# Performance work log

Measured on AMD Instinct MI355X. Metric: run time of the kernel, lower is better.

Reference implementation:

```python
import jax, jax.numpy as jnp
import numpy as np

CPS = 16          # coarse_patch_size = 128 / resolution[0](=8)
ENC = 128         # enc_dim = CPS*CPS/2
LN_EPS = 1e-5


def setup_inputs() -> dict:
    key = jax.random.key(0)
    ks = jax.random.split(key, 10)
    B, C, H, W = 4, 256, 160, 160
    s = 0.05
    return {
        "feat_c1": jax.random.normal(ks[0], (B, C, H, W), dtype=jnp.float32),
        "feat_c2": jax.random.normal(ks[1], (B, C, H, W), dtype=jnp.float32),
        "mask_c1": jnp.ones((1, H, W), dtype=bool),
        "img_conv_w": jax.random.normal(ks[2], (1, C), dtype=jnp.float32) * s,
        "img_conv_b": jnp.zeros((1,), jnp.float32),
        "img_w1": jax.random.normal(ks[3], (2 * ENC, 2 * ENC), dtype=jnp.float32) * s,
        "img_w2": jax.random.normal(ks[4], (ENC, 2 * ENC), dtype=jnp.float32) * s,
        "img_ln_g": jnp.ones((ENC,), jnp.float32),
        "img_ln_b": jnp.zeros((ENC,), jnp.float32),
        "depth_conv_w": jax.random.normal(ks[5], (1, C), dtype=jnp.float32) * s,
        "depth_conv_b": jnp.zeros((1,), jnp.float32),
        "depth_w1": jax.random.normal(ks[6], (2 * ENC, 2 * ENC), dtype=jnp.float32) * s,
        "depth_w2": jax.random.normal(ks[7], (ENC, 2 * ENC), dtype=jnp.float32) * s,
        "depth_ln_g": jnp.ones((ENC,), jnp.float32),
        "depth_ln_b": jnp.zeros((ENC,), jnp.float32),
        "logit_scale": jnp.asarray(np.log(1.0 / 0.07), jnp.float32),
    }


def _grid_from_mask(mask_c1):
    # replicate get_patches: grid size from max lit row/col of the mask
    m = np.asarray(mask_c1)[0]
    inds = np.argwhere(m)
    feat_h = int(inds[:, 0].max()) + 1
    feat_w = int(inds[:, 1].max()) + 1
    nv = int(feat_w / CPS + 0.5)   # outer loop count (row starts), as in source
    nh = int(feat_h / CPS + 0.5)   # inner loop count (col starts)
    return nv, nh


def _extract_patches(feat, nv, nh):
    # vectorized equivalent of the nested python-loop gather: non-overlapping
    # CPS x CPS tiles, row-major order matching (r outer, c inner)
    B, C = feat.shape[0], feat.shape[1]
    f = feat[:, :, : nv * CPS, : nh * CPS]
    f = f.reshape(B, C, nv, CPS, nh, CPS)
    f = f.transpose(0, 2, 4, 1, 3, 5)          # [B, nv, nh, C, CPS, CPS]
    return f.reshape(B * nv * nh, C, CPS, CPS)


def _branch(patches, conv_w, conv_b, w1, w2, ln_g, ln_b):
    # conv1x1 (256 -> 1) + ReLU
    x = jnp.einsum("bchw,oc->bohw", patches, conv_w) + conv_b[None, :, None, None]
    x = jax.nn.relu(x)
    x = x.reshape(x.shape[0], -1)              # [B*N, 2*ENC]
    # Linear(no bias) -> ReLU -> Linear(no bias)
    x = jax.nn.relu(x @ w1.T) @ w2.T           # [B*N, ENC]
    mu = jnp.mean(x, axis=-1, keepdims=True)
    var = jnp.var(x, axis=-1, keepdims=True)
    return (x - mu) / jnp.sqrt(var + LN_EPS) * ln_g + ln_b


def reference(feat_c1, feat_c2, mask_c1, img_conv_w, img_conv_b, img_w1, img_w2,
              img_ln_g, img_ln_b, depth_conv_w, depth_conv_b, depth_w1, depth_w2,
              depth_ln_g, depth_ln_b, logit_scale):
    nv, nh = _grid_from_mask(mask_c1)
    N = nv * nh
    B = feat_c1.shape[0]
    p1 = _extract_patches(feat_c1, nv, nh)
    p2 = _extract_patches(feat_c2, nv, nh)
    e1 = _branch(p1, img_conv_w, img_conv_b, img_w1, img_w2, img_ln_g, img_ln_b)
    e2 = _branch(p2, depth_conv_w, depth_conv_b, depth_w1, depth_w2, depth_ln_g, depth_ln_b)
    e1 = e1.reshape(B, N, ENC)
    e2 = e2.reshape(B, N, ENC)
    scale = jnp.exp(logit_scale)
    logits_per_img = scale * jnp.einsum("bnd,bmd->bnm", e1, e2)   # [B, N, N]
    logits_per_depth = jnp.swapaxes(logits_per_img, 1, 2)
    return logits_per_img, logits_per_depth
```

## Files before the change

kernel.cpp:

```cpp
#include <hip/hip_runtime.h>
#include <math.h>

#define CPS 16
#define ENC 128
#define NH 10
#define NPATCH 100
#define BATCH 4
#define CCH 256
#define WIDTH 160
#define HW 25600
#define ROWS_TOTAL 400

__global__ __launch_bounds__(64) void conv_relu_kernel(
    const float* __restrict__ f1, const float* __restrict__ f2,
    const float* __restrict__ wci, const float* __restrict__ bci,
    const float* __restrict__ wcd, const float* __restrict__ bcd,
    float* __restrict__ xr)
{
    int tid   = threadIdx.x;
    int plane = blockIdx.x / 200;
    int wb    = blockIdx.x % 200;
    int branch = plane >> 2;
    int b      = plane & 3;

    const float* f    = branch ? f2  : f1;
    const float* wsel = branch ? wcd : wci;
    float bias        = branch ? bcd[0] : bci[0];

    int pp  = wb * 64 + tid;
    int pix = pp * 2;

    const float* fbase = f + (size_t)b * CCH * HW + pix;
    float2 acc = make_float2(0.f, 0.f);
    #pragma unroll 8
    for (int c = 0; c < CCH; ++c) {
        float2 v = *(const float2*)(fbase + (size_t)c * HW);
        float wc = wsel[c];
        acc.x = fmaf(v.x, wc, acc.x);
        acc.y = fmaf(v.y, wc, acc.y);
    }
    acc.x = fmaxf(acc.x + bias, 0.f);
    acc.y = fmaxf(acc.y + bias, 0.f);

    int h = pix / WIDTH, w = pix % WIDTH;
    int p = b * NPATCH + (h >> 4) * NH + (w >> 4);
    int j = (h & 15) * CPS + (w & 15);
    *(float2*)(xr + ((size_t)(branch * ROWS_TOTAL + p)) * 256 + j) = acc;
}

__global__ __launch_bounds__(256) void mlp_ln_kernel(
    const float* __restrict__ xr,
    const float* __restrict__ w1i, const float* __restrict__ w2i,
    const float* __restrict__ gi,  const float* __restrict__ bli,
    const float* __restrict__ w1d, const float* __restrict__ w2d,
    const float* __restrict__ gd,  const float* __restrict__ bld,
    float* __restrict__ e)
{
    const int R = 4;
    __shared__ float xs[R][256];
    __shared__ float ys[R][256];
    __shared__ float zs[R][ENC];

    int tid    = threadIdx.x;
    int branch = blockIdx.x / 100;
    int row0   = (blockIdx.x % 100) * R;

    const float* w1 = branch ? w1d : w1i;
    const float* w2 = branch ? w2d : w2i;
    const float* g  = branch ? gd  : gi;
    const float* bl = branch ? bld : bli;

    #pragma unroll
    for (int r = 0; r < R; ++r)
        xs[r][tid] = xr[((size_t)(branch * ROWS_TOTAL + row0 + r)) * 256 + tid];
    __syncthreads();

    {
        float acc[R] = {0.f, 0.f, 0.f, 0.f};
        const float4* w1r = (const float4*)(w1 + (size_t)tid * 256);
        #pragma unroll 4
        for (int c4 = 0; c4 < 64; ++c4) {
            float4 wv = w1r[c4];
            #pragma unroll
            for (int r = 0; r < R; ++r) {
                float4 xv = *(const float4*)(&xs[r][c4 * 4]);
                acc[r] = fmaf(xv.x, wv.x, acc[r]);
                acc[r] = fmaf(xv.y, wv.y, acc[r]);
                acc[r] = fmaf(xv.z, wv.z, acc[r]);
                acc[r] = fmaf(xv.w, wv.w, acc[r]);
            }
        }
        #pragma unroll
        for (int r = 0; r < R; ++r) ys[r][tid] = fmaxf(acc[r], 0.f);
    }
    __syncthreads();

    #pragma unroll
    for (int i = 0; i < 2; ++i) {
        int idx = tid + 256 * i;
        int r = idx >> 7, m = idx & 127;
        float acc = 0.f;
        const float4* w2r = (const float4*)(w2 + (size_t)m * 256);
        #pragma unroll 4
        for (int c4 = 0; c4 < 64; ++c4) {
            float4 wv = w2r[c4];
            float4 yv = *(const float4*)(&ys[r][c4 * 4]);
            acc = fmaf(yv.x, wv.x, acc);
            acc = fmaf(yv.y, wv.y, acc);
            acc = fmaf(yv.z, wv.z, acc);
            acc = fmaf(yv.w, wv.w, acc);
        }
        zs[r][m] = acc;
    }
    __syncthreads();

    int r = tid >> 6, lane = tid & 63;
    float a  = zs[r][lane];
    float b2 = zs[r][lane + 64];
    float s = a + b2;
    float q = a * a + b2 * b2;
    #pragma unroll
    for (int off = 32; off >= 1; off >>= 1) {
        s += __shfl_xor(s, off);
        q += __shfl_xor(q, off);
    }
    float mu  = s * (1.f / 128.f);
    float var = q * (1.f / 128.f) - mu * mu;
    float inv = 1.f / sqrtf(var + 1e-5f);
    float* erow = e + ((size_t)(branch * ROWS_TOTAL + row0 + r)) * ENC;
    erow[lane]      = (a  - mu) * inv * g[lane]      + bl[lane];
    erow[lane + 64] = (b2 - mu) * inv * g[lane + 64] + bl[lane + 64];
}

__global__ __launch_bounds__(256) void logits_kernel(
    const float* __restrict__ e, const float* __restrict__ lsc,
    float* __restrict__ out)
{
    int gidx = blockIdx.x * 256 + threadIdx.x;
    if (gidx >= BATCH * NPATCH * NPATCH) return;
    float scale = expf(lsc[0]);

    int b    = gidx / (NPATCH * NPATCH);
    int rrem = gidx % (NPATCH * NPATCH);
    int n = rrem / NPATCH, m = rrem % NPATCH;

    const float4* e1 = (const float4*)(e + (size_t)(b * NPATCH + n) * ENC);
    const float4* e2 = (const float4*)(e + (size_t)(ROWS_TOTAL + b * NPATCH + m) * ENC);
    float acc = 0.f;
    #pragma unroll 8
    for (int c4 = 0; c4 < ENC / 4; ++c4) {
        float4 av = e1[c4], bv = e2[c4];
        acc = fmaf(av.x, bv.x, acc);
        acc = fmaf(av.y, bv.y, acc);
        acc = fmaf(av.z, bv.z, acc);
        acc = fmaf(av.w, bv.w, acc);
    }
    float L = scale * acc;
    out[gidx] = L;
    out[BATCH * NPATCH * NPATCH + b * NPATCH * NPATCH + m * NPATCH + n] = L;
}

extern "C" void kernel_launch(void* const* d_in, const int* in_sizes, int n_in,
                              void* d_out, int out_size, void* d_ws, size_t ws_size,
                              hipStream_t stream) {
    const float* f1  = (const float*)d_in[0];
    const float* f2  = (const float*)d_in[1];
    const float* wci = (const float*)d_in[3];
    const float* bci = (const float*)d_in[4];
    const float* w1i = (const float*)d_in[5];
    const float* w2i = (const float*)d_in[6];
    const float* gi  = (const float*)d_in[7];
    const float* bli = (const float*)d_in[8];
    const float* wcd = (const float*)d_in[9];
    const float* bcd = (const float*)d_in[10];
    const float* w1d = (const float*)d_in[11];
    const float* w2d = (const float*)d_in[12];
    const float* gd  = (const float*)d_in[13];
    const float* bld = (const float*)d_in[14];
    const float* lsc = (const float*)d_in[15];

    float* xr = (float*)d_ws;
    float* e  = xr + 2 * ROWS_TOTAL * 256;
    float* out = (float*)d_out;

    conv_relu_kernel<<<1600, 64, 0, stream>>>(f1, f2, wci, bci, wcd, bcd, xr);
    mlp_ln_kernel<<<200, 256, 0, stream>>>(xr, w1i, w2i, gi, bli,
                                           w1d, w2d, gd, bld, e);
    logits_kernel<<<(BATCH * NPATCH * NPATCH + 255) / 256, 256, 0, stream>>>(e, lsc, out);
}
```

Baseline: 285.9 us.

## Split conv channel reduction across blocks with atomic partial sums

The 1x1 conv now splits the 256 channels into 16 groups handled by separate blocks. Each block reads float4 vectors covering 5 pixel groups per thread and accumulates partial sums into a zeroed workspace with atomicAdd. Bias, ReLU and the patch gather move into the MLP kernel's load stage. This aims to expose more parallelism and memory-level concurrency for the bandwidth-bound channel sweep, at the cost of an extra memset, atomic traffic and a non-deterministic summation order.

New measurement: 315.8 us. 1.1x slower.

```diff
diff --git a/kernel.cpp b/kernel.cpp
--- a/kernel.cpp
+++ b/kernel.cpp
@@ -11,45 +11,57 @@
 #define HW 25600
 #define ROWS_TOTAL 400
 
-__global__ __launch_bounds__(64) void conv_relu_kernel(
+__global__ __launch_bounds__(256) void conv_partial_kernel(
     const float* __restrict__ f1, const float* __restrict__ f2,
-    const float* __restrict__ wci, const float* __restrict__ bci,
-    const float* __restrict__ wcd, const float* __restrict__ bcd,
-    float* __restrict__ xr)
+    const float* __restrict__ wci, const float* __restrict__ wcd,
+    float* __restrict__ partial)
 {
-    int tid   = threadIdx.x;
-    int plane = blockIdx.x / 200;
-    int wb    = blockIdx.x % 200;
+    int lane = threadIdx.x & 63;
+    int wv   = threadIdx.x >> 6;
+
+    int bid   = blockIdx.x;
+    int cg    = bid & 15;
+    int rest  = bid >> 4;
+    int plane = rest & 7;
+    int pxc   = rest >> 3;
     int branch = plane >> 2;
     int b      = plane & 3;
 
     const float* f    = branch ? f2  : f1;
     const float* wsel = branch ? wcd : wci;
-    float bias        = branch ? bcd[0] : bci[0];
-
-    int pp  = wb * 64 + tid;
-    int pix = pp * 2;
-
-    const float* fbase = f + (size_t)b * CCH * HW + pix;
-    float2 acc = make_float2(0.f, 0.f);
-    #pragma unroll 8
-    for (int c = 0; c < CCH; ++c) {
-        float2 v = *(const float2*)(fbase + (size_t)c * HW);
-        float wc = wsel[c];
-        acc.x = fmaf(v.x, wc, acc.x);
-        acc.y = fmaf(v.y, wc, acc.y);
-    }
-    acc.x = fmaxf(acc.x + bias, 0.f);
-    acc.y = fmaxf(acc.y + bias, 0.f);
-
-    int h = pix / WIDTH, w = pix % WIDTH;
-    int p = b * NPATCH + (h >> 4) * NH + (w >> 4);
-    int j = (h & 15) * CPS + (w & 15);
-    *(float2*)(xr + ((size_t)(branch * ROWS_TOTAL + p)) * 256 + j) = acc;
+    int c0 = cg * 16;
+
+    int pxbase = pxc * 5120 + wv * 1280 + lane * 4;
+    const float* fb = f + ((size_t)(b * CCH + c0)) * HW + pxbase;
+
+    float4 acc[5] = {};
+    #pragma unroll 4
+    for (int c = 0; c < 16; ++c) {
+        float wc = wsel[c0 + c];
+        const float* p = fb + (size_t)c * HW;
+        #pragma unroll
+        for (int j = 0; j < 5; ++j) {
+            float4 v = *(const float4*)(p + j * 256);
+            acc[j].x = fmaf(v.x, wc, acc[j].x);
+            acc[j].y = fmaf(v.y, wc, acc[j].y);
+            acc[j].z = fmaf(v.z, wc, acc[j].z);
+            acc[j].w = fmaf(v.w, wc, acc[j].w);
+        }
+    }
+
+    float* pp = partial + (size_t)plane * HW + pxbase;
+    #pragma unroll
+    for (int j = 0; j < 5; ++j) {
+        atomicAdd(pp + j * 256 + 0, acc[j].x);
+        atomicAdd(pp + j * 256 + 1, acc[j].y);
+        atomicAdd(pp + j * 256 + 2, acc[j].z);
+        atomicAdd(pp + j * 256 + 3, acc[j].w);
+    }
 }
 
 __global__ __launch_bounds__(256) void mlp_ln_kernel(
-    const float* __restrict__ xr,
+    const float* __restrict__ partial,
+    const float* __restrict__ bci,  const float* __restrict__ bcd,
     const float* __restrict__ w1i, const float* __restrict__ w2i,
     const float* __restrict__ gi,  const float* __restrict__ bli,
     const float* __restrict__ w1d, const float* __restrict__ w2d,
@@ -69,10 +81,21 @@
     const float* w2 = branch ? w2d : w2i;
     const float* g  = branch ? gd  : gi;
     const float* bl = branch ? bld : bli;
-
-    #pragma unroll
-    for (int r = 0; r < R; ++r)
-        xs[r][tid] = xr[((size_t)(branch * ROWS_TOTAL + row0 + r)) * 256 + tid];
+    float bias      = branch ? bcd[0] : bci[0];
+
+    {
+        int hh = tid >> 4, ww = tid & 15;
+        #pragma unroll
+        for (int r = 0; r < R; ++r) {
+            int prow  = row0 + r;
+            int b     = prow / 100;
+            int patch = prow % 100;
+            int pv = patch / 10, ph = patch % 10;
+            int pixel = (pv * 16 + hh) * WIDTH + ph * 16 + ww;
+            float v = partial[(size_t)(branch * BATCH + b) * HW + pixel] + bias;
+            xs[r][tid] = fmaxf(v, 0.f);
+        }
+    }
     __syncthreads();
 
     {
@@ -179,12 +202,15 @@
     const float* bld = (const float*)d_in[14];
     const float* lsc = (const float*)d_in[15];
 
-    float* xr = (float*)d_ws;
-    float* e  = xr + 2 * ROWS_TOTAL * 256;
+    float* partial = (float*)d_ws;
+    float* e       = partial + 2 * BATCH * HW;
     float* out = (float*)d_out;
 
-    conv_relu_kernel<<<1600, 64, 0, stream>>>(f1, f2, wci, bci, wcd, bcd, xr);
-    mlp_ln_kernel<<<200, 256, 0, stream>>>(xr, w1i, w2i, gi, bli,
+    hipMemsetAsync(partial, 0, (size_t)2 * BATCH * HW * sizeof(float), stream);
+
+    conv_partial_kernel<<<640, 256, 0, stream>>>(f1, f2, wci, wcd, partial);
+    mlp_ln_kernel<<<200, 256, 0, stream>>>(partial, bci, bcd,
+                                           w1i, w2i, gi, bli,
                                            w1d, w2d, gd, bld, e);
     logits_kernel<<<(BATCH * NPATCH * NPATCH + 255) / 256, 256, 0, stream>>>(e, lsc, out);
 }
```
